# Kernel tuning notes

Measured on AMD Instinct MI355X. Metric: run time of the kernel, lower is better.

The kernel has to match this reference:

```python
import jax, jax.numpy as jnp
import numpy as np
from jax import lax

HIDDEN_DIM = 32
MLP_INNER = 8
VOCAB_SIZE = 64
INFERENCE_LR = 0.01
THRESHOLD = 4.0
B, L = 256, 4096
LN_EPS = 1e-5


def setup_inputs() -> dict:
    key = jax.random.key(0)
    ks = jax.random.split(key, 14)
    s = 0.1
    f32 = jnp.float32
    return {
        "seq": jax.random.randint(ks[0], (B, L), 0, VOCAB_SIZE),
        "embed": (jax.random.normal(ks[1], (VOCAB_SIZE, HIDDEN_DIM)) * s).astype(f32),
        "ff1_w": (jax.random.normal(ks[2], (2 * HIDDEN_DIM, HIDDEN_DIM)) * s).astype(f32),
        "ff1_b": jnp.zeros((2 * HIDDEN_DIM,), f32),
        "ff2_w": (jax.random.normal(ks[3], (HIDDEN_DIM, 2 * HIDDEN_DIM)) * s).astype(f32),
        "ff2_b": jnp.zeros((HIDDEN_DIM,), f32),
        "ln_g": jnp.ones((HIDDEN_DIM,), f32),
        "ln_b": jnp.zeros((HIDDEN_DIM,), f32),
        "fc1_w": (jax.random.normal(ks[4], (MLP_INNER, HIDDEN_DIM)) * s).astype(f32),
        "fc1_b": jnp.zeros((MLP_INNER,), f32),
        "fc2_w": (jax.random.normal(ks[5], (HIDDEN_DIM, MLP_INNER)) * s).astype(f32),
        "fc2_b": jnp.zeros((HIDDEN_DIM,), f32),
        "out_w": (jax.random.normal(ks[6], (VOCAB_SIZE, HIDDEN_DIM)) * s).astype(f32),
        "out_b": jnp.zeros((VOCAB_SIZE,), f32),
    }


def _encoder(seq, embed, ff1_w, ff1_b, ff2_w, ff2_b, ln_g, ln_b):
    h = embed[seq]  # [B, L, H]
    z = jax.nn.relu(jnp.einsum('blh,kh->blk', h, ff1_w) + ff1_b)
    f = jnp.einsum('blk,hk->blh', z, ff2_w) + ff2_b
    x = h + f
    mu = x.mean(-1, keepdims=True)
    var = ((x - mu) ** 2).mean(-1, keepdims=True)
    return ln_g * (x - mu) * lax.rsqrt(var + LN_EPS) + ln_b


def _fast_weight_scan(keys, vals, query, fc1_w, fc1_b, fc2_w, fc2_b):
    # keys, vals: [n_steps, H] for one sample; query: [H]
    H = keys.shape[-1]

    def step(carry, kv):
        W1, b1, W2, b2, ssum, cnt = carry
        k, v = kv
        mean_h = ssum / jnp.maximum(cnt, 1.0)
        dist = jnp.sqrt(jnp.sum((k - mean_h) ** 2))
        write = jnp.logical_or(cnt == 0.0, dist > THRESHOLD)
        # forward of tiny MLP on key
        z1 = W1 @ k + b1
        a = jax.nn.relu(z1)
        pred = W2 @ a + b2
        # MSE (mean over H) gradient, manual SGD step
        dpred = (2.0 / H) * (pred - v)
        dW2 = jnp.outer(dpred, a)
        db2 = dpred
        dz1 = (W2.T @ dpred) * (z1 > 0)
        dW1 = jnp.outer(dz1, k)
        db1 = dz1
        lr = INFERENCE_LR
        W1n = jnp.where(write, W1 - lr * dW1, W1)
        b1n = jnp.where(write, b1 - lr * db1, b1)
        W2n = jnp.where(write, W2 - lr * dW2, W2)
        b2n = jnp.where(write, b2 - lr * db2, b2)
        return (W1n, b1n, W2n, b2n, ssum + k, cnt + 1.0), write

    carry0 = (fc1_w, fc1_b, fc2_w, fc2_b, jnp.zeros_like(query), jnp.asarray(0.0, query.dtype))
    (W1, b1, W2, b2, _, _), writes = lax.scan(step, carry0, (keys, vals))
    context = W2 @ jax.nn.relu(W1 @ query + b1) + b2
    return context, writes.sum()


def reference(seq, embed, ff1_w, ff1_b, ff2_w, ff2_b, ln_g, ln_b,
              fc1_w, fc1_b, fc2_w, fc2_b, out_w, out_b):
    hidden = _encoder(seq, embed, ff1_w, ff1_b, ff2_w, ff2_b, ln_g, ln_b)
    hidden = lax.stop_gradient(hidden)  # inner loop uses detached hiddens
    Lseq = hidden.shape[1]
    n = (Lseq - 3 + 1) // 2  # len(range(0, L-3, 2))
    keys = hidden[:, 0:2 * n:2, :]   # [B, n, H]
    vals = hidden[:, 1:2 * n:2, :]   # [B, n, H]
    query = hidden[:, -1, :]          # [B, H]
    ctx, n_writes = jax.vmap(_fast_weight_scan, in_axes=(0, 0, 0, None, None, None, None))(
        keys, vals, query, fc1_w, fc1_b, fc2_w, fc2_b)
    ctx = lax.stop_gradient(ctx)  # torch computes context under no_grad
    logits = ctx @ out_w.T + out_b  # [B, VOCAB]
    write_rate = n_writes.sum().astype(jnp.float32) / (hidden.shape[0] * n)
    return logits, write_rate
```

## Files before the change

kernel.cpp:

```cpp
#include <hip/hip_runtime.h>

#define L_SEQ 4096
#define NSTEP 2047
#define LR 0.01f

__device__ __forceinline__ void redi4(float& a, float& b, float& c, float& d) {
    asm volatile(
        "s_nop 1\n\t"
        "v_add_f32_dpp %0, %0, %0 quad_perm:[1,0,3,2] row_mask:0xf bank_mask:0xf bound_ctrl:0\n\t"
        "v_add_f32_dpp %1, %1, %1 quad_perm:[1,0,3,2] row_mask:0xf bank_mask:0xf bound_ctrl:0\n\t"
        "v_add_f32_dpp %2, %2, %2 quad_perm:[1,0,3,2] row_mask:0xf bank_mask:0xf bound_ctrl:0\n\t"
        "v_add_f32_dpp %3, %3, %3 quad_perm:[1,0,3,2] row_mask:0xf bank_mask:0xf bound_ctrl:0\n\t"
        "v_add_f32_dpp %0, %0, %0 quad_perm:[2,3,0,1] row_mask:0xf bank_mask:0xf bound_ctrl:0\n\t"
        "v_add_f32_dpp %1, %1, %1 quad_perm:[2,3,0,1] row_mask:0xf bank_mask:0xf bound_ctrl:0\n\t"
        "v_add_f32_dpp %2, %2, %2 quad_perm:[2,3,0,1] row_mask:0xf bank_mask:0xf bound_ctrl:0\n\t"
        "v_add_f32_dpp %3, %3, %3 quad_perm:[2,3,0,1] row_mask:0xf bank_mask:0xf bound_ctrl:0\n\t"
        "v_add_f32_dpp %0, %0, %0 row_half_mirror row_mask:0xf bank_mask:0xf bound_ctrl:0\n\t"
        "v_add_f32_dpp %1, %1, %1 row_half_mirror row_mask:0xf bank_mask:0xf bound_ctrl:0\n\t"
        "v_add_f32_dpp %2, %2, %2 row_half_mirror row_mask:0xf bank_mask:0xf bound_ctrl:0\n\t"
        "v_add_f32_dpp %3, %3, %3 row_half_mirror row_mask:0xf bank_mask:0xf bound_ctrl:0"
        : "+v"(a), "+v"(b), "+v"(c), "+v"(d));
}

__device__ __forceinline__ void redg2(float& x, float& y) {
    float t0, t1;
    asm volatile(
        "s_nop 1\n\t"
        "v_add_f32_dpp %0, %0, %0 row_ror:8 row_mask:0xf bank_mask:0xf bound_ctrl:0\n\t"
        "v_add_f32_dpp %1, %1, %1 row_ror:8 row_mask:0xf bank_mask:0xf bound_ctrl:0\n\t"
        "v_mov_b32 %2, %0\n\t"
        "v_mov_b32 %3, %1\n\t"
        "s_nop 0\n\t"
        "v_permlane16_swap_b32 %2, %0\n\t"
        "v_permlane16_swap_b32 %3, %1\n\t"
        "v_add_f32 %0, %0, %2\n\t"
        "v_add_f32 %1, %1, %3\n\t"
        "v_mov_b32 %2, %0\n\t"
        "v_mov_b32 %3, %1\n\t"
        "s_nop 0\n\t"
        "v_permlane32_swap_b32 %2, %0\n\t"
        "v_permlane32_swap_b32 %3, %1\n\t"
        "v_add_f32 %0, %0, %2\n\t"
        "v_add_f32 %1, %1, %3"
        : "+v"(x), "+v"(y), "=&v"(t0), "=&v"(t1));
}

__device__ __forceinline__ float redg1(float x) {
    float t;
    asm volatile(
        "s_nop 1\n\t"
        "v_add_f32_dpp %0, %0, %0 row_ror:8 row_mask:0xf bank_mask:0xf bound_ctrl:0\n\t"
        "s_nop 1\n\t"
        "v_mov_b32 %1, %0\n\t"
        "s_nop 1\n\t"
        "v_permlane16_swap_b32 %1, %0\n\t"
        "s_nop 0\n\t"
        "v_add_f32 %0, %0, %1\n\t"
        "s_nop 1\n\t"
        "v_mov_b32 %1, %0\n\t"
        "s_nop 1\n\t"
        "v_permlane32_swap_b32 %1, %0\n\t"
        "s_nop 0\n\t"
        "v_add_f32 %0, %0, %1"
        : "+v"(x), "=&v"(t));
    return x;
}

__global__ __launch_bounds__(64) void build_table_kernel(
    const float* __restrict__ embed, const float* __restrict__ ff1_w,
    const float* __restrict__ ff1_b, const float* __restrict__ ff2_w,
    const float* __restrict__ ff2_b, const float* __restrict__ ln_g,
    const float* __restrict__ ln_b, float* __restrict__ table)
{
    const int v = threadIdx.x;
    float h[32], f[32];
#pragma unroll
    for (int j = 0; j < 32; ++j) { h[j] = embed[v * 32 + j]; f[j] = 0.f; }
    for (int k = 0; k < 64; ++k) {
        float z = ff1_b[k];
#pragma unroll
        for (int j = 0; j < 32; ++j) z += h[j] * ff1_w[k * 32 + j];
        z = fmaxf(z, 0.f);
#pragma unroll
        for (int j = 0; j < 32; ++j) f[j] += z * ff2_w[j * 64 + k];
    }
    float x[32], mu = 0.f;
#pragma unroll
    for (int j = 0; j < 32; ++j) { x[j] = h[j] + f[j] + ff2_b[j]; mu += x[j]; }
    mu *= (1.f / 32.f);
    float var = 0.f;
#pragma unroll
    for (int j = 0; j < 32; ++j) { float d = x[j] - mu; var += d * d; }
    var *= (1.f / 32.f);
    const float inv = rsqrtf(var + 1e-5f);
#pragma unroll
    for (int j = 0; j < 32; ++j)
        table[v * 32 + j] = ln_g[j] * (x[j] - mu) * inv + ln_b[j];
}

__global__ __launch_bounds__(64) void scan_kernel(
    const int* __restrict__ seq, const float* __restrict__ table_g,
    const float* __restrict__ fc1_w, const float* __restrict__ fc1_b,
    const float* __restrict__ fc2_w, const float* __restrict__ fc2_b,
    const float* __restrict__ out_w, const float* __restrict__ out_b,
    float* __restrict__ out, float* __restrict__ wacc)
{
    __shared__ float tab[64][32];
    __shared__ float ctx_s[32];
    const int b   = blockIdx.x;
    const int tid = threadIdx.x;
    const int i   = tid & 7;
    const int g   = tid >> 3;

    for (int idx = tid; idx < 2048; idx += 64)
        (&tab[0][0])[idx] = table_g[idx];
    __syncthreads();

    float4 W1r = reinterpret_cast<const float4*>(fc1_w)[i * 8 + g];
    float  b1  = fc1_b[i];
    float  W2r0 = fc2_w[(4 * g + 0) * 8 + i];
    float  W2r1 = fc2_w[(4 * g + 1) * 8 + i];
    float  W2r2 = fc2_w[(4 * g + 2) * 8 + i];
    float  W2r3 = fc2_w[(4 * g + 3) * 8 + i];
    float4 b2r = reinterpret_cast<const float4*>(fc2_b)[g];
    float4 ssum = make_float4(0.f, 0.f, 0.f, 0.f);
    float  nw = 0.f;
    float  cntf = 0.f;

    const int2* srow = reinterpret_cast<const int2*>(seq + b * L_SEQ);
    const float4* tab4 = reinterpret_cast<const float4*>(&tab[0][0]);

    int2 tkb = srow[1];
    {
        int2 tka = srow[0];
        (void)tka;
    }
    int2 tka0 = srow[0];
    float4 kc = tab4[tka0.x * 8 + g];
    float4 vc = tab4[tka0.y * 8 + g];

#pragma unroll 2
    for (int t = 0; t < NSTEP; ++t) {
        int2 tkc = srow[(t + 2 < 2048) ? (t + 2) : 2047];
        float4 kn = tab4[tkb.x * 8 + g];
        float4 vn = tab4[tkb.y * 8 + g];

        const float cntm = fmaxf(cntf, 1.0f);
        const float mrc  = -__builtin_amdgcn_rcpf(cntm);
        float d0 = fmaf(ssum.x, mrc, kc.x);
        float d1 = fmaf(ssum.y, mrc, kc.y);
        float d2 = fmaf(ssum.z, mrc, kc.z);
        float d3 = fmaf(ssum.w, mrc, kc.w);
        float dd = (d0 * d0 + d1 * d1) + (d2 * d2 + d3 * d3);

        float zp = W1r.x * kc.x + W1r.y * kc.y + W1r.z * kc.z + W1r.w * kc.w;

        redg2(dd, zp);

        const bool wr = (cntf == 0.0f) || (dd > 16.0f);
        const float z1 = zp + b1;
        const float a  = fmaxf(z1, 0.f);

        const float es0 = (b2r.x - vc.x) * 0.0625f;
        const float es1 = (b2r.y - vc.y) * 0.0625f;
        const float es2 = (b2r.z - vc.z) * 0.0625f;
        const float es3 = (b2r.w - vc.w) * 0.0625f;

        float p0 = W2r0 * a, p1 = W2r1 * a, p2 = W2r2 * a, p3 = W2r3 * a;
        redi4(p0, p1, p2, p3);
        const float dp0 = fmaf(p0, 0.0625f, es0);
        const float dp1 = fmaf(p1, 0.0625f, es1);
        const float dp2 = fmaf(p2, 0.0625f, es2);
        const float dp3 = fmaf(p3, 0.0625f, es3);

        float qa = fmaf(W2r0, dp0, W2r1 * dp1);
        float qb = fmaf(W2r2, dp2, W2r3 * dp3);
        float q  = redg1(qa + qb);
        const float dz1 = (z1 > 0.f) ? q : 0.f;

        if (wr) {
            const float v1 = -LR * dz1;
            W1r.x = fmaf(v1, kc.x, W1r.x); W1r.y = fmaf(v1, kc.y, W1r.y);
            W1r.z = fmaf(v1, kc.z, W1r.z); W1r.w = fmaf(v1, kc.w, W1r.w);
            b1 += v1;
            const float u0 = -LR * dp0, u1 = -LR * dp1, u2 = -LR * dp2, u3 = -LR * dp3;
            W2r0 = fmaf(u0, a, W2r0); W2r1 = fmaf(u1, a, W2r1);
            W2r2 = fmaf(u2, a, W2r2); W2r3 = fmaf(u3, a, W2r3);
            b2r.x += u0; b2r.y += u1; b2r.z += u2; b2r.w += u3;
            nw += 1.f;
        }
        ssum.x += kc.x; ssum.y += kc.y; ssum.z += kc.z; ssum.w += kc.w;
        cntf += 1.0f;
        kc = kn; vc = vn; tkb = tkc;
    }

    const int tq = seq[b * L_SEQ + (L_SEQ - 1)];
    float4 kq = tab4[tq * 8 + g];
    float zq = W1r.x * kq.x + W1r.y * kq.y + W1r.z * kq.z + W1r.w * kq.w;
    zq = redg1(zq);
    const float aq = fmaxf(zq + b1, 0.f);
    float c0 = W2r0 * aq, c1 = W2r1 * aq, c2 = W2r2 * aq, c3 = W2r3 * aq;
    redi4(c0, c1, c2, c3);
    if (i == 0) {
        ctx_s[4 * g + 0] = c0 + b2r.x;
        ctx_s[4 * g + 1] = c1 + b2r.y;
        ctx_s[4 * g + 2] = c2 + b2r.z;
        ctx_s[4 * g + 3] = c3 + b2r.w;
    }
    __syncthreads();

    float acc = out_b[tid];
#pragma unroll
    for (int j = 0; j < 32; ++j) acc += ctx_s[j] * out_w[tid * 32 + j];
    out[b * 64 + tid] = acc;

    if (tid == 0) atomicAdd(wacc, nw);
}

__global__ void finalize_kernel(const float* __restrict__ wacc,
                                float* __restrict__ out)
{
    out[16384] = wacc[0] / 524032.0f;
}

extern "C" void kernel_launch(void* const* d_in, const int* in_sizes, int n_in,
                              void* d_out, int out_size, void* d_ws, size_t ws_size,
                              hipStream_t stream)
{
    const int*   seq   = (const int*)  d_in[0];
    const float* embed = (const float*)d_in[1];
    const float* ff1_w = (const float*)d_in[2];
    const float* ff1_b = (const float*)d_in[3];
    const float* ff2_w = (const float*)d_in[4];
    const float* ff2_b = (const float*)d_in[5];
    const float* ln_g  = (const float*)d_in[6];
    const float* ln_b  = (const float*)d_in[7];
    const float* fc1_w = (const float*)d_in[8];
    const float* fc1_b = (const float*)d_in[9];
    const float* fc2_w = (const float*)d_in[10];
    const float* fc2_b = (const float*)d_in[11];
    const float* out_w = (const float*)d_in[12];
    const float* out_b = (const float*)d_in[13];

    float* out   = (float*)d_out;
    float* table = (float*)d_ws;
    float* wacc  = (float*)((char*)d_ws + 8192);

    hipMemsetAsync(wacc, 0, sizeof(float), stream);
    hipLaunchKernelGGL(build_table_kernel, dim3(1), dim3(64), 0, stream,
                       embed, ff1_w, ff1_b, ff2_w, ff2_b, ln_g, ln_b, table);
    hipLaunchKernelGGL(scan_kernel, dim3(256), dim3(64), 0, stream,
                       seq, table, fc1_w, fc1_b, fc2_w, fc2_b,
                       out_w, out_b, out, wacc);
    hipLaunchKernelGGL(finalize_kernel, dim3(1), dim3(1), 0, stream, wacc, out);
}
```

Before: 521.1 us.

## Precompute Gram matrix and write flags, track W1 via token-space Z

Precomputes a 64x64 Gram matrix of the normalized embedding table and the fc1 projection of every token. A separate flags kernel works out the write/skip decisions from Gram-matrix recurrences instead of 32-dim distance reductions. The scan then keeps W1 implicitly as per-token preactivations Z, updated with rank-1 Gram rows, which removes the W1·k reduction and the distance reduction from the serial critical path. This costs an extra kernel pass over the sequence, a 16KB shared Gram table per block, and different floating-point rounding in the threshold test near the boundary.

```diff
diff --git a/kernel.cpp b/kernel.cpp
--- a/kernel.cpp
+++ b/kernel.cpp
@@ -2,7 +2,8 @@
 
 #define L_SEQ 4096
 #define NSTEP 2047
-#define LR 0.01f
+#define ST_W  (-0.000625f)
+
 
 __device__ __forceinline__ void redi4(float& a, float& b, float& c, float& d) {
     asm volatile(
@@ -22,29 +23,6 @@
         : "+v"(a), "+v"(b), "+v"(c), "+v"(d));
 }
 
-__device__ __forceinline__ void redg2(float& x, float& y) {
-    float t0, t1;
-    asm volatile(
-        "s_nop 1\n\t"
-        "v_add_f32_dpp %0, %0, %0 row_ror:8 row_mask:0xf bank_mask:0xf bound_ctrl:0\n\t"
-        "v_add_f32_dpp %1, %1, %1 row_ror:8 row_mask:0xf bank_mask:0xf bound_ctrl:0\n\t"
-        "v_mov_b32 %2, %0\n\t"
-        "v_mov_b32 %3, %1\n\t"
-        "s_nop 0\n\t"
-        "v_permlane16_swap_b32 %2, %0\n\t"
-        "v_permlane16_swap_b32 %3, %1\n\t"
-        "v_add_f32 %0, %0, %2\n\t"
-        "v_add_f32 %1, %1, %3\n\t"
-        "v_mov_b32 %2, %0\n\t"
-        "v_mov_b32 %3, %1\n\t"
-        "s_nop 0\n\t"
-        "v_permlane32_swap_b32 %2, %0\n\t"
-        "v_permlane32_swap_b32 %3, %1\n\t"
-        "v_add_f32 %0, %0, %2\n\t"
-        "v_add_f32 %1, %1, %3"
-        : "+v"(x), "+v"(y), "=&v"(t0), "=&v"(t1));
-}
-
 __device__ __forceinline__ float redg1(float x) {
     float t;
     asm volatile(
@@ -66,12 +44,29 @@
     return x;
 }
 
-__global__ __launch_bounds__(64) void build_table_kernel(
+__device__ __forceinline__ float sel8(const float* Z, int r) {
+    float a0 = (r & 1) ? Z[1] : Z[0];
+    float a1 = (r & 1) ? Z[3] : Z[2];
+    float a2 = (r & 1) ? Z[5] : Z[4];
+    float a3 = (r & 1) ? Z[7] : Z[6];
+    float b0 = (r & 2) ? a1 : a0;
+    float b1_ = (r & 2) ? a3 : a2;
+    return (r & 4) ? b1_ : b0;
+}
+
+__device__ __forceinline__ float bperm_row(int tok, int i, float v) {
+    int addr = (((tok & 56) | i) << 2);
+    return __int_as_float(__builtin_amdgcn_ds_bpermute(addr, __float_as_int(v)));
+}
+
+__global__ __launch_bounds__(64) void build_kernel(
     const float* __restrict__ embed, const float* __restrict__ ff1_w,
     const float* __restrict__ ff1_b, const float* __restrict__ ff2_w,
     const float* __restrict__ ff2_b, const float* __restrict__ ln_g,
-    const float* __restrict__ ln_b, float* __restrict__ table)
-{
+    const float* __restrict__ ln_b, const float* __restrict__ fc1_w,
+    float* __restrict__ table, float* __restrict__ G, float* __restrict__ Z0)
+{
+    __shared__ float tl[64][32];
     const int v = threadIdx.x;
     float h[32], f[32];
 #pragma unroll
@@ -93,112 +88,151 @@
     for (int j = 0; j < 32; ++j) { float d = x[j] - mu; var += d * d; }
     var *= (1.f / 32.f);
     const float inv = rsqrtf(var + 1e-5f);
-#pragma unroll
-    for (int j = 0; j < 32; ++j)
-        table[v * 32 + j] = ln_g[j] * (x[j] - mu) * inv + ln_b[j];
+    float tv[32];
+#pragma unroll
+    for (int j = 0; j < 32; ++j) {
+        tv[j] = ln_g[j] * (x[j] - mu) * inv + ln_b[j];
+        tl[v][j] = tv[j];
+        table[v * 32 + j] = tv[j];
+    }
+    __syncthreads();
+    for (int u = 0; u < 64; ++u) {
+        float acc = 0.f;
+#pragma unroll
+        for (int j = 0; j < 32; ++j) acc += tv[j] * tl[u][j];
+        G[v * 64 + u] = acc;
+    }
+    for (int i = 0; i < 8; ++i) {
+        float acc = 0.f;
+#pragma unroll
+        for (int j = 0; j < 32; ++j) acc += fc1_w[i * 32 + j] * tv[j];
+        Z0[v * 8 + i] = acc;
+    }
+}
+
+__global__ __launch_bounds__(64) void flags_kernel(
+    const int* __restrict__ seq, const float* __restrict__ Gg,
+    unsigned int* __restrict__ flags, unsigned int* __restrict__ wacc)
+{
+    __shared__ float Gs[4096];
+    const int v = threadIdx.x, b = blockIdx.x;
+    for (int idx = v; idx < 4096; idx += 64) Gs[idx] = Gg[idx];
+    __syncthreads();
+    const int* sp = seq + b * L_SEQ;
+    unsigned int* frow = flags + b * 64;
+
+    float S = 0.f, u = 0.f, tf = 0.f;
+    unsigned int word = 0, cnt = 0;
+
+    int tok  = sp[0];
+    int tok1 = sp[2];
+    float grow = Gs[tok * 64 + v];
+
+    for (int t = 0; t < NSTEP; ++t) {
+        int tok2 = sp[(2 * t + 4) & 4095];
+        float grow1 = Gs[tok1 * 64 + v];
+        float A   = __int_as_float(__builtin_amdgcn_readlane(__float_as_int(S), tok));
+        float Gtt = __int_as_float(__builtin_amdgcn_readlane(__float_as_int(grow), tok));
+        float r = fmaf(tf * tf, Gtt - 16.f, u) - 2.f * tf * A;
+        bool wr = (t == 0) || (r > 0.f);
+        word |= (wr ? 1u : 0u) << (t & 31);
+        if ((t & 31) == 31) { frow[t >> 5] = word; cnt += __popc(word); word = 0; }
+        u += 2.f * A + Gtt;
+        S += grow;
+        tf += 1.f;
+        grow = grow1; tok = tok1; tok1 = tok2;
+    }
+    frow[63] = word; cnt += __popc(word);
+    if (v == 0) atomicAdd(wacc, cnt);
 }
 
 __global__ __launch_bounds__(64) void scan_kernel(
-    const int* __restrict__ seq, const float* __restrict__ table_g,
-    const float* __restrict__ fc1_w, const float* __restrict__ fc1_b,
-    const float* __restrict__ fc2_w, const float* __restrict__ fc2_b,
-    const float* __restrict__ out_w, const float* __restrict__ out_b,
-    float* __restrict__ out, float* __restrict__ wacc)
-{
-    __shared__ float tab[64][32];
+    const int* __restrict__ seq, const float* __restrict__ tableg,
+    const float* __restrict__ Gg, const float* __restrict__ Z0g,
+    const float* __restrict__ fc1_b, const float* __restrict__ fc2_w,
+    const float* __restrict__ fc2_b, const float* __restrict__ out_w,
+    const float* __restrict__ out_b, const unsigned int* __restrict__ flags,
+    float* __restrict__ out)
+{
+    __shared__ float Gs[4096];
+    __shared__ float tabs[2048];
     __shared__ float ctx_s[32];
-    const int b   = blockIdx.x;
-    const int tid = threadIdx.x;
-    const int i   = tid & 7;
-    const int g   = tid >> 3;
-
-    for (int idx = tid; idx < 2048; idx += 64)
-        (&tab[0][0])[idx] = table_g[idx];
-    __syncthreads();
-
-    float4 W1r = reinterpret_cast<const float4*>(fc1_w)[i * 8 + g];
-    float  b1  = fc1_b[i];
-    float  W2r0 = fc2_w[(4 * g + 0) * 8 + i];
-    float  W2r1 = fc2_w[(4 * g + 1) * 8 + i];
-    float  W2r2 = fc2_w[(4 * g + 2) * 8 + i];
-    float  W2r3 = fc2_w[(4 * g + 3) * 8 + i];
+    const int b = blockIdx.x, tid = threadIdx.x;
+    const int i = tid & 7, g = tid >> 3;
+    for (int idx = tid; idx < 4096; idx += 64) Gs[idx] = Gg[idx];
+    for (int idx = tid; idx < 2048; idx += 64) tabs[idx] = tableg[idx];
+    __syncthreads();
+    const float4* tab4 = reinterpret_cast<const float4*>(tabs);
+
+    float Zr[8];
+#pragma unroll
+    for (int r = 0; r < 8; ++r) Zr[r] = Z0g[(8 * g + r) * 8 + i];
+    float b1 = fc1_b[i];
+    float W2r0 = fc2_w[(4 * g + 0) * 8 + i];
+    float W2r1 = fc2_w[(4 * g + 1) * 8 + i];
+    float W2r2 = fc2_w[(4 * g + 2) * 8 + i];
+    float W2r3 = fc2_w[(4 * g + 3) * 8 + i];
     float4 b2r = reinterpret_cast<const float4*>(fc2_b)[g];
-    float4 ssum = make_float4(0.f, 0.f, 0.f, 0.f);
-    float  nw = 0.f;
-    float  cntf = 0.f;
-
-    const int2* srow = reinterpret_cast<const int2*>(seq + b * L_SEQ);
-    const float4* tab4 = reinterpret_cast<const float4*>(&tab[0][0]);
-
-    int2 tkb = srow[1];
-    {
-        int2 tka = srow[0];
-        (void)tka;
-    }
-    int2 tka0 = srow[0];
-    float4 kc = tab4[tka0.x * 8 + g];
-    float4 vc = tab4[tka0.y * 8 + g];
+
+    const int* sp = seq + b * L_SEQ;
+    const unsigned int* frow = flags + b * 64;
+
+    int tokk  = sp[0], tokv  = sp[1];
+    int tokk1 = sp[2], tokv1 = sp[3];
+    const float4* gr0 = reinterpret_cast<const float4*>(Gs + tokk * 64 + 8 * g);
+    float4 Ga = gr0[0], Gb = gr0[1];
+    float y_pre = bperm_row(tokk, i, sel8(Zr, tokk & 7));
+    float Gx = 0.f, c_prev = 0.f;
+    float4 vc = tab4[tokv * 8 + g];
+    unsigned int fw = frow[0];
 
 #pragma unroll 2
     for (int t = 0; t < NSTEP; ++t) {
-        int2 tkc = srow[(t + 2 < 2048) ? (t + 2) : 2047];
-        float4 kn = tab4[tkb.x * 8 + g];
-        float4 vn = tab4[tkb.y * 8 + g];
-
-        const float cntm = fmaxf(cntf, 1.0f);
-        const float mrc  = -__builtin_amdgcn_rcpf(cntm);
-        float d0 = fmaf(ssum.x, mrc, kc.x);
-        float d1 = fmaf(ssum.y, mrc, kc.y);
-        float d2 = fmaf(ssum.z, mrc, kc.z);
-        float d3 = fmaf(ssum.w, mrc, kc.w);
-        float dd = (d0 * d0 + d1 * d1) + (d2 * d2 + d3 * d3);
-
-        float zp = W1r.x * kc.x + W1r.y * kc.y + W1r.z * kc.z + W1r.w * kc.w;
-
-        redg2(dd, zp);
-
-        const bool wr = (cntf == 0.0f) || (dd > 16.0f);
-        const float z1 = zp + b1;
+        if ((t & 31) == 0) fw = frow[t >> 5];
+        int tokk2 = sp[(2 * t + 4) & 4095];
+        int tokv2 = sp[(2 * t + 5) & 4095];
+        const float st = ((fw >> (t & 31)) & 1) ? ST_W : 0.0f;
+
+        const float4* grn = reinterpret_cast<const float4*>(Gs + tokk1 * 64 + 8 * g);
+        float4 Gan = grn[0], Gbn = grn[1];
+        float Gxn = Gs[tokk * 64 + tokk1];
+        float4 vcn = tab4[tokv1 * 8 + g];
+
+        const float y2 = y_pre + b1;
+        const float z1 = fmaf(c_prev, Gx, y2);
         const float a  = fmaxf(z1, 0.f);
 
-        const float es0 = (b2r.x - vc.x) * 0.0625f;
-        const float es1 = (b2r.y - vc.y) * 0.0625f;
-        const float es2 = (b2r.z - vc.z) * 0.0625f;
-        const float es3 = (b2r.w - vc.w) * 0.0625f;
+        float ysel = sel8(Zr, tokk1 & 7);
+        float y_pre_n = bperm_row(tokk1, i, ysel);
 
         float p0 = W2r0 * a, p1 = W2r1 * a, p2 = W2r2 * a, p3 = W2r3 * a;
         redi4(p0, p1, p2, p3);
-        const float dp0 = fmaf(p0, 0.0625f, es0);
-        const float dp1 = fmaf(p1, 0.0625f, es1);
-        const float dp2 = fmaf(p2, 0.0625f, es2);
-        const float dp3 = fmaf(p3, 0.0625f, es3);
-
-        float qa = fmaf(W2r0, dp0, W2r1 * dp1);
-        float qb = fmaf(W2r2, dp2, W2r3 * dp3);
-        float q  = redg1(qa + qb);
-        const float dz1 = (z1 > 0.f) ? q : 0.f;
-
-        if (wr) {
-            const float v1 = -LR * dz1;
-            W1r.x = fmaf(v1, kc.x, W1r.x); W1r.y = fmaf(v1, kc.y, W1r.y);
-            W1r.z = fmaf(v1, kc.z, W1r.z); W1r.w = fmaf(v1, kc.w, W1r.w);
-            b1 += v1;
-            const float u0 = -LR * dp0, u1 = -LR * dp1, u2 = -LR * dp2, u3 = -LR * dp3;
-            W2r0 = fmaf(u0, a, W2r0); W2r1 = fmaf(u1, a, W2r1);
-            W2r2 = fmaf(u2, a, W2r2); W2r3 = fmaf(u3, a, W2r3);
-            b2r.x += u0; b2r.y += u1; b2r.z += u2; b2r.w += u3;
-            nw += 1.f;
-        }
-        ssum.x += kc.x; ssum.y += kc.y; ssum.z += kc.z; ssum.w += kc.w;
-        cntf += 1.0f;
-        kc = kn; vc = vn; tkb = tkc;
-    }
-
-    const int tq = seq[b * L_SEQ + (L_SEQ - 1)];
-    float4 kq = tab4[tq * 8 + g];
-    float zq = W1r.x * kq.x + W1r.y * kq.y + W1r.z * kq.z + W1r.w * kq.w;
-    zq = redg1(zq);
-    const float aq = fmaxf(zq + b1, 0.f);
+        const float dp0 = p0 + (b2r.x - vc.x);
+        const float dp1 = p1 + (b2r.y - vc.y);
+        const float dp2 = p2 + (b2r.z - vc.z);
+        const float dp3 = p3 + (b2r.w - vc.w);
+        float q = redg1(fmaf(W2r0, dp0, W2r1 * dp1) + fmaf(W2r2, dp2, W2r3 * dp3));
+        const float c = (z1 > 0.f) ? st * q : 0.f;
+
+        const float u0 = st * dp0, u1 = st * dp1, u2 = st * dp2, u3 = st * dp3;
+        W2r0 = fmaf(u0, a, W2r0); W2r1 = fmaf(u1, a, W2r1);
+        W2r2 = fmaf(u2, a, W2r2); W2r3 = fmaf(u3, a, W2r3);
+        b2r.x += u0; b2r.y += u1; b2r.z += u2; b2r.w += u3;
+        b1 += c;
+        Zr[0] = fmaf(c, Ga.x, Zr[0]); Zr[1] = fmaf(c, Ga.y, Zr[1]);
+        Zr[2] = fmaf(c, Ga.z, Zr[2]); Zr[3] = fmaf(c, Ga.w, Zr[3]);
+        Zr[4] = fmaf(c, Gb.x, Zr[4]); Zr[5] = fmaf(c, Gb.y, Zr[5]);
+        Zr[6] = fmaf(c, Gb.z, Zr[6]); Zr[7] = fmaf(c, Gb.w, Zr[7]);
+
+        y_pre = y_pre_n; Gx = Gxn; c_prev = c;
+        Ga = Gan; Gb = Gbn; vc = vcn;
+        tokk = tokk1; tokv = tokv1; tokk1 = tokk2; tokv1 = tokv2;
+    }
+
+    const int tq = sp[L_SEQ - 1];
+    float yq = bperm_row(tq, i, sel8(Zr, tq & 7));
+    const float zq = yq + b1;
+    const float aq = fmaxf(zq, 0.f);
     float c0 = W2r0 * aq, c1 = W2r1 * aq, c2 = W2r2 * aq, c3 = W2r3 * aq;
     redi4(c0, c1, c2, c3);
     if (i == 0) {
@@ -213,14 +247,12 @@
 #pragma unroll
     for (int j = 0; j < 32; ++j) acc += ctx_s[j] * out_w[tid * 32 + j];
     out[b * 64 + tid] = acc;
-
-    if (tid == 0) atomicAdd(wacc, nw);
-}
-
-__global__ void finalize_kernel(const float* __restrict__ wacc,
+}
+
+__global__ void finalize_kernel(const unsigned int* __restrict__ wacc,
                                 float* __restrict__ out)
 {
-    out[16384] = wacc[0] / 524032.0f;
+    out[16384] = (float)(*wacc) / 524032.0f;
 }
 
 extern "C" void kernel_launch(void* const* d_in, const int* in_sizes, int n_in,
@@ -242,15 +274,22 @@
     const float* out_w = (const float*)d_in[12];
     const float* out_b = (const float*)d_in[13];
 
-    float* out   = (float*)d_out;
-    float* table = (float*)d_ws;
-    float* wacc  = (float*)((char*)d_ws + 8192);
-
-    hipMemsetAsync(wacc, 0, sizeof(float), stream);
-    hipLaunchKernelGGL(build_table_kernel, dim3(1), dim3(64), 0, stream,
-                       embed, ff1_w, ff1_b, ff2_w, ff2_b, ln_g, ln_b, table);
+    float* out = (float*)d_out;
+    char* ws = (char*)d_ws;
+    float*        table = (float*)(ws + 0);
+    float*        G     = (float*)(ws + 8192);
+    float*        Z0    = (float*)(ws + 24576);
+    unsigned int* wacc  = (unsigned int*)(ws + 26624);
+    unsigned int* flags = (unsigned int*)(ws + 28672);
+
+    hipMemsetAsync(wacc, 0, sizeof(unsigned int), stream);
+    hipLaunchKernelGGL(build_kernel, dim3(1), dim3(64), 0, stream,
+                       embed, ff1_w, ff1_b, ff2_w, ff2_b, ln_g, ln_b, fc1_w,
+                       table, G, Z0);
+    hipLaunchKernelGGL(flags_kernel, dim3(256), dim3(64), 0, stream,
+                       seq, G, flags, wacc);
     hipLaunchKernelGGL(scan_kernel, dim3(256), dim3(64), 0, stream,
-                       seq, table, fc1_w, fc1_b, fc2_w, fc2_b,
-                       out_w, out_b, out, wacc);
+                       seq, table, G, Z0, fc1_b, fc2_w, fc2_b,
+                       out_w, out_b, flags, out);
     hipLaunchKernelGGL(finalize_kernel, dim3(1), dim3(1), 0, stream, wacc, out);
 }
```

Result: slower. 638.6 us (+22.6%).
